# Kernel tuning notes

Measured on AMD Instinct MI355X. Metric: run time of the kernel, lower is better.

The kernel has to match this reference:

```python
import jax, jax.numpy as jnp
import numpy as np

EPS = 1e-5

def layernorm(x, g, b):
    mu = jnp.mean(x, axis=-1, keepdims=True)
    var = jnp.mean((x - mu) ** 2, axis=-1, keepdims=True)
    return (x - mu) * jax.lax.rsqrt(var + EPS) * g + b

def setup_inputs() -> dict:
    key = jax.random.key(0)
    B, T, C, H = 4, 2048, 1024, 16
    hs = C // H  # 64
    ks = jax.random.split(key, 16)
    s_in = 1.0 / np.sqrt(C)
    s_hid = 1.0 / np.sqrt(4 * C)
    return {
        "x":   jax.random.normal(ks[0], (B, T, C), jnp.float32),
        # per-head projections, stacked over heads: [H, C, hs]
        "Wq":  jax.random.normal(ks[1], (H, C, hs), jnp.float32) * s_in,
        "Wk":  jax.random.normal(ks[2], (H, C, hs), jnp.float32) * s_in,
        "Wv":  jax.random.normal(ks[3], (H, C, hs), jnp.float32) * s_in,
        # output projection [C, C] (concat of heads -> C)
        "Wo":  jax.random.normal(ks[4], (C, C), jnp.float32) * s_in,
        "bo":  jnp.zeros((C,), jnp.float32),
        # layernorm params
        "g1":  jnp.ones((C,), jnp.float32),
        "be1": jnp.zeros((C,), jnp.float32),
        "g2":  jnp.ones((C,), jnp.float32),
        "be2": jnp.zeros((C,), jnp.float32),
        # feed-forward: C -> 4C -> C
        "W1":  jax.random.normal(ks[5], (C, 4 * C), jnp.float32) * s_in,
        "b1":  jnp.zeros((4 * C,), jnp.float32),
        "W2":  jax.random.normal(ks[6], (4 * C, C), jnp.float32) * s_hid,
        "b2":  jnp.zeros((C,), jnp.float32),
    }

def reference(x, Wq, Wk, Wv, Wo, bo, g1, be1, g2, be2, W1, b1, W2, b2):
    B, T, C = x.shape
    H, _, hs = Wq.shape
    scale = hs ** -0.5

    # --- self-attention on ln1(x) ---
    xn = layernorm(x, g1, be1)
    q = jnp.einsum('btc,hcd->bhtd', xn, Wq)
    k = jnp.einsum('btc,hcd->bhtd', xn, Wk)
    v = jnp.einsum('btc,hcd->bhtd', xn, Wv)
    scores = jnp.einsum('bhtd,bhsd->bhts', q, k) * scale  # [B,H,T,T]
    causal = jnp.tril(jnp.ones((T, T), dtype=bool))
    scores = jnp.where(causal, scores, jnp.finfo(scores.dtype).min)
    wei = jax.nn.softmax(scores, axis=-1)
    out = jnp.einsum('bhts,bhsd->bhtd', wei, v)           # [B,H,T,hs]
    out = out.transpose(0, 2, 1, 3).reshape(B, T, H * hs)  # concat heads
    x = x + out @ Wo + bo

    # --- feed-forward on ln2(x) ---
    xn2 = layernorm(x, g2, be2)
    h = jax.nn.relu(xn2 @ W1 + b1)
    x = x + h @ W2 + b2
    return x
```

## Files before the change

### kernel.cpp

```cpp
#include <hip/hip_runtime.h>
#include <hip/hip_bf16.h>

typedef __hip_bfloat16 bf16;
typedef __attribute__((ext_vector_type(8))) short bf16x8;
typedef __attribute__((ext_vector_type(4))) short s16x4;
typedef __attribute__((ext_vector_type(4))) float f32x4;

__device__ __forceinline__ float b2f(bf16 v) { return __bfloat162float(v); }
__device__ __forceinline__ bf16  f2b(float v) { return __float2bfloat16(v); }
__device__ __forceinline__ float ldf(const bf16* p)  { return __bfloat162float(*p); }
__device__ __forceinline__ float ldf(const float* p) { return *p; }
__device__ __forceinline__ void  stf(bf16* p, float v)  { *p = __float2bfloat16(v); }
__device__ __forceinline__ void  stf(float* p, float v) { *p = v; }

__device__ __forceinline__ void load_lds16(const bf16* g, short* lds) {
    __builtin_amdgcn_global_load_lds(
        (const __attribute__((address_space(1))) unsigned int*)g,
        (__attribute__((address_space(3))) unsigned int*)lds, 16, 0, 0);
}

template<typename InT>
__global__ __launch_bounds__(256) void ln_kernel(const InT* __restrict__ x,
                                                 const float* __restrict__ g,
                                                 const float* __restrict__ b,
                                                 bf16* __restrict__ out)
{
    const int C = 1024;
    int row = blockIdx.x;
    int tid = threadIdx.x;
    const InT* xr = x + (size_t)row * C;

    float v[4];
    float s = 0.f, s2 = 0.f;
#pragma unroll
    for (int i = 0; i < 4; ++i) {
        float f = ldf(xr + tid + i * 256);
        v[i] = f; s += f; s2 += f * f;
    }
#pragma unroll
    for (int off = 32; off > 0; off >>= 1) {
        s  += __shfl_down(s,  off, 64);
        s2 += __shfl_down(s2, off, 64);
    }
    __shared__ float red[8];
    int wave = tid >> 6;
    if ((tid & 63) == 0) { red[wave] = s; red[wave + 4] = s2; }
    __syncthreads();
    float ts  = red[0] + red[1] + red[2] + red[3];
    float ts2 = red[4] + red[5] + red[6] + red[7];
    float mu  = ts * (1.f / 1024.f);
    float var = ts2 * (1.f / 1024.f) - mu * mu;
    float rstd = rsqrtf(var + 1e-5f);
#pragma unroll
    for (int i = 0; i < 4; ++i) {
        int c = tid + i * 256;
        out[(size_t)row * C + c] = f2b((v[i] - mu) * rstd * g[c] + b[c]);
    }
}

__global__ __launch_bounds__(256) void prep_weights(
    const float* __restrict__ Wq, const float* __restrict__ Wk,
    const float* __restrict__ Wv, const float* __restrict__ Wo,
    const float* __restrict__ W1, const float* __restrict__ W2,
    bf16* __restrict__ wqkvt, bf16* __restrict__ wot,
    bf16* __restrict__ w1t, bf16* __restrict__ w2t)
{
    __shared__ float t[32][33];
    int tx = threadIdx.x & 31, ty = threadIdx.x >> 5;
    int id = blockIdx.x;
    const float* in; bf16* out; int in_ld, out_ld, n0, k0;
    if (id < 3072) {
        const float* Ws[3] = {Wq, Wk, Wv};
        int m = id >> 10, r = id & 1023;
        int z = r >> 6, rt = r & 63;
        in = Ws[m] + z * 65536;
        out = wqkvt + (size_t)(m * 1024 + z * 64) * 1024;
        in_ld = 64; out_ld = 1024;
        n0 = (rt & 1) * 32; k0 = (rt >> 1) * 32;
    } else if (id < 4096) {
        int r = id - 3072;
        in = Wo; out = wot; in_ld = 1024; out_ld = 1024;
        n0 = (r & 31) * 32; k0 = (r >> 5) * 32;
    } else if (id < 8192) {
        int r = id - 4096;
        in = W1; out = w1t; in_ld = 4096; out_ld = 1024;
        n0 = (r & 127) * 32; k0 = (r >> 7) * 32;
    } else {
        int r = id - 8192;
        in = W2; out = w2t; in_ld = 1024; out_ld = 4096;
        n0 = (r & 31) * 32; k0 = (r >> 5) * 32;
    }
#pragma unroll
    for (int i = 0; i < 4; ++i)
        t[ty + i * 8][tx] = in[(size_t)(k0 + ty + i * 8) * in_ld + n0 + tx];
    __syncthreads();
#pragma unroll
    for (int i = 0; i < 4; ++i)
        out[(size_t)(n0 + ty + i * 8) * out_ld + k0 + tx] = f2b(t[tx][ty + i * 8]);
}

__global__ __launch_bounds__(256) void vt_kernel(
    const bf16* __restrict__ qkv, bf16* __restrict__ vt, int T)
{
    __shared__ float t[32][33];
    int tx = threadIdx.x & 31, ty = threadIdx.x >> 5;
    int z = blockIdx.z, b = z >> 4, h = z & 15;
    const bf16* in = qkv + (size_t)b * T * 3072 + 2048 + h * 64;
    bf16* out = vt + (size_t)z * 64 * T;
    int n0 = blockIdx.x * 32, k0 = blockIdx.y * 32;
#pragma unroll
    for (int i = 0; i < 4; ++i)
        t[ty + i * 8][tx] = b2f(in[(size_t)(k0 + ty + i * 8) * 3072 + n0 + tx]);
    __syncthreads();
#pragma unroll
    for (int i = 0; i < 4; ++i)
        out[(size_t)(n0 + ty + i * 8) * T + k0 + tx] = f2b(t[tx][ty + i * 8]);
}

template<bool RELU, bool HAS_BIAS, bool HAS_RES, typename ResT, typename OutT>
__global__ __launch_bounds__(256) void gemm_bt(
    const bf16* __restrict__ A, int lda,
    const bf16* __restrict__ Bt, int ldb,
    const float* __restrict__ bias,
    const ResT* __restrict__ res, int ldr,
    OutT* __restrict__ Cm, int ldc,
    int M, int N, int K)
{
    __shared__ short As[2][128 * 32];
    __shared__ short Bs[2][128 * 32];
    int tid = threadIdx.x, wv = tid >> 6, ln = tid & 63;

    int f = blockIdx.x + blockIdx.y * gridDim.x;
    int nby = gridDim.y;
    int by = f % nby, bx = f / nby;
    int bm0 = by * 128, bn0 = bx * 128;

    int wm = (wv & 1) * 64, wn = (wv >> 1) * 64;
    int quad = ln >> 4, lane15 = ln & 15;

    f32x4 acc[4][4] = {};

    int srow = ln >> 2;
    int scol = (((ln & 3) ^ (srow & 3)) * 8);
    int sw   = (quad ^ (lane15 & 3)) * 8;
    const bf16* Ab = A + (size_t)bm0 * lda;
    const bf16* Bb = Bt + (size_t)bn0 * ldb;

#pragma unroll
    for (int i = 0; i < 2; ++i) {
        int ch = wv + i * 4;
        load_lds16(Ab + (size_t)(ch * 16 + srow) * lda + scol, &As[0][ch * 16 * 32]);
        load_lds16(Bb + (size_t)(ch * 16 + srow) * ldb + scol, &Bs[0][ch * 16 * 32]);
    }
    __syncthreads();

    int cur = 0;
    for (int k0 = 0; k0 < K; k0 += 32) {
        if (k0 + 32 < K) {
            int nb = cur ^ 1;
#pragma unroll
            for (int i = 0; i < 2; ++i) {
                int ch = wv + i * 4;
                load_lds16(Ab + (size_t)(ch * 16 + srow) * lda + k0 + 32 + scol,
                           &As[nb][ch * 16 * 32]);
                load_lds16(Bb + (size_t)(ch * 16 + srow) * ldb + k0 + 32 + scol,
                           &Bs[nb][ch * 16 * 32]);
            }
        }
        bf16x8 af[4], bfr[4];
#pragma unroll
        for (int mi = 0; mi < 4; ++mi)
            af[mi] = *(const bf16x8*)&As[cur][(wm + mi * 16 + lane15) * 32 + sw];
#pragma unroll
        for (int ni = 0; ni < 4; ++ni)
            bfr[ni] = *(const bf16x8*)&Bs[cur][(wn + ni * 16 + lane15) * 32 + sw];
#pragma unroll
        for (int mi = 0; mi < 4; ++mi)
#pragma unroll
            for (int ni = 0; ni < 4; ++ni)
                acc[mi][ni] = __builtin_amdgcn_mfma_f32_16x16x32_bf16(
                    af[mi], bfr[ni], acc[mi][ni], 0, 0, 0);
        __syncthreads();
        cur ^= 1;
    }

#pragma unroll
    for (int mi = 0; mi < 4; ++mi) {
#pragma unroll
        for (int r = 0; r < 4; ++r) {
            int gm = bm0 + wm + mi * 16 + quad * 4 + r;
#pragma unroll
            for (int ni = 0; ni < 4; ++ni) {
                int gn = bn0 + wn + ni * 16 + lane15;
                float v = acc[mi][ni][r];
                if (HAS_BIAS) v += bias[gn];
                if (HAS_RES)  v += ldf(res + (size_t)gm * ldr + gn);
                if (RELU)     v = fmaxf(v, 0.f);
                stf(Cm + (size_t)gm * ldc + gn, v);
            }
        }
    }
}

__device__ __forceinline__ void attn_tile_q(
    const short* __restrict__ Ks, const short* __restrict__ Vs,
    short* __restrict__ Psw,
    const bf16x8* qf, f32x4* oacc, float& mrun, float& lrun,
    int ktbase, int qmin, int quad, int lane15, int r7)
{
    const float scale2 = 0.18033688011112042f;
    const int PS = 72;
    f32x4 sacc[4] = {};
    __builtin_amdgcn_s_setprio(1);
#pragma unroll
    for (int ks = 0; ks < 2; ++ks) {
        int so = ((ks * 4 + quad) ^ r7) * 8;
#pragma unroll
        for (int mi = 0; mi < 4; ++mi) {
            bf16x8 kf = *(const bf16x8*)&Ks[(mi * 16 + lane15) * 64 + so];
            sacc[mi] = __builtin_amdgcn_mfma_f32_16x16x32_bf16(kf, qf[ks], sacc[mi], 0, 0, 0);
        }
    }
    __builtin_amdgcn_s_setprio(0);

    if (ktbase + 63 > qmin) {
        int ql = qmin + lane15;
#pragma unroll
        for (int mi = 0; mi < 4; ++mi)
#pragma unroll
            for (int r = 0; r < 4; ++r)
                if (ktbase + mi * 16 + quad * 4 + r > ql) sacc[mi][r] = -3e38f;
    }

    float mx = sacc[0][0];
#pragma unroll
    for (int mi = 0; mi < 4; ++mi)
#pragma unroll
        for (int r = 0; r < 4; ++r) mx = fmaxf(mx, sacc[mi][r]);
    mx = fmaxf(mx, __shfl_xor(mx, 16, 64));
    mx = fmaxf(mx, __shfl_xor(mx, 32, 64));
    float pmax = mx * scale2;

    if (!__all(pmax <= mrun + 11.5f)) {
        float mn = fmaxf(mrun, pmax);
        float alpha = exp2f(mrun - mn);
        mrun = mn;
        lrun *= alpha;
#pragma unroll
        for (int di = 0; di < 4; ++di)
#pragma unroll
            for (int r = 0; r < 4; ++r) oacc[di][r] *= alpha;
    }

    float psum = 0.f;
#pragma unroll
    for (int mi = 0; mi < 4; ++mi) {
        float p[4];
#pragma unroll
        for (int r = 0; r < 4; ++r) {
            p[r] = exp2f(fmaf(sacc[mi][r], scale2, -mrun));
            psum += p[r];
        }
        short tmp[4];
#pragma unroll
        for (int r = 0; r < 4; ++r) {
            bf16 pb = f2b(p[r]);
            tmp[r] = *(short*)&pb;
        }
        *(s16x4*)&Psw[lane15 * PS + mi * 16 + quad * 4] = *(s16x4*)tmp;
    }
    lrun += psum;

    __builtin_amdgcn_s_setprio(1);
#pragma unroll
    for (int ks = 0; ks < 2; ++ks) {
        int so = ((ks * 4 + quad) ^ r7) * 8;
        bf16x8 pf = *(const bf16x8*)&Psw[lane15 * PS + ks * 32 + quad * 8];
#pragma unroll
        for (int di = 0; di < 4; ++di) {
            bf16x8 vf = *(const bf16x8*)&Vs[(di * 16 + lane15) * 64 + so];
            oacc[di] = __builtin_amdgcn_mfma_f32_16x16x32_bf16(vf, pf, oacc[di], 0, 0, 0);
        }
    }
    __builtin_amdgcn_s_setprio(0);
}

__global__ __launch_bounds__(512, 4) void attn_kernel(
    const bf16* __restrict__ qkv, const bf16* __restrict__ vt,
    bf16* __restrict__ o, int T)
{
    const int LDQ = 3072;
    const int PS = 72;
    int bx = blockIdx.x;
    int qta = 15 - bx;
    int qtb = bx;
    int h = blockIdx.y, b = blockIdx.z;
    int tid = threadIdx.x, wv = tid >> 6, ln = tid & 63;
    int quad = ln >> 4, lane15 = ln & 15, r7 = lane15 & 7;

    __shared__ short KV[2][2][64 * 64];
    __shared__ short Ps[2][8][16 * PS];

    int lr = ln >> 3;
    int lc = ((ln & 7) ^ lr) * 8;

    const bf16* kbase = qkv + (size_t)(b * T) * LDQ + 1024 + h * 64;
    const bf16* vbase = vt + (size_t)((b * 16 + h) * 64) * T;

#pragma unroll
    for (int i = 0; i < 2; ++i) {
        int ch = wv * 2 + i;
        load_lds16(qkv + (size_t)(b * T + qta * 128 + ch * 8 + lr) * LDQ + h * 64 + lc,
                   &KV[0][0][ch * 512]);
        load_lds16(qkv + (size_t)(b * T + qtb * 128 + ch * 8 + lr) * LDQ + h * 64 + lc,
                   &KV[1][0][ch * 512]);
    }
    __syncthreads();
    bf16x8 qfa[2], qfb[2];
#pragma unroll
    for (int ks = 0; ks < 2; ++ks) {
        int off = (wv * 16 + lane15) * 64 + (((ks * 4 + quad) ^ r7) * 8);
        qfa[ks] = *(const bf16x8*)&KV[0][0][off];
        qfb[ks] = *(const bf16x8*)&KV[1][0][off];
    }
    __syncthreads();

    f32x4 oacca[4] = {}, oaccb[4] = {};
    float mra = -1e30f, lra = 0.f, mrb = -1e30f, lrb = 0.f;
    int qmina = qta * 128 + wv * 16;
    int qminb = qtb * 128 + wv * 16;
    int ntiles = 2 * qta + 2;

    load_lds16(kbase + (size_t)(wv * 8 + lr) * LDQ + lc, &KV[0][0][wv * 8 * 64]);
    load_lds16(vbase + (size_t)(wv * 8 + lr) * T + lc, &KV[0][1][wv * 8 * 64]);

    for (int kt = 0; kt < ntiles; ++kt) {
        __syncthreads();
        if (kt + 1 < ntiles) {
            int nb = (kt + 1) & 1;
            load_lds16(kbase + (size_t)((kt + 1) * 64 + wv * 8 + lr) * LDQ + lc,
                       &KV[nb][0][wv * 8 * 64]);
            load_lds16(vbase + (size_t)(wv * 8 + lr) * T + (kt + 1) * 64 + lc,
                       &KV[nb][1][wv * 8 * 64]);
        }
        const short* Ks = &KV[kt & 1][0][0];
        const short* Vs = &KV[kt & 1][1][0];
        int kb = kt * 64;

        if (kb <= qmina + 15)
            attn_tile_q(Ks, Vs, &Ps[0][wv][0], qfa, oacca, mra, lra,
                        kb, qmina, quad, lane15, r7);
        if (kb <= qminb + 15)
            attn_tile_q(Ks, Vs, &Ps[1][wv][0], qfb, oaccb, mrb, lrb,
                        kb, qminb, quad, lane15, r7);
    }

    lra += __shfl_xor(lra, 16, 64);
    lra += __shfl_xor(lra, 32, 64);
    float inva = 1.f / lra;
    size_t rowa = (size_t)(b * T + qta * 128 + wv * 16 + lane15);
#pragma unroll
    for (int di = 0; di < 4; ++di) {
        short tmp[4];
#pragma unroll
        for (int r = 0; r < 4; ++r) {
            bf16 ob = f2b(oacca[di][r] * inva);
            tmp[r] = *(short*)&ob;
        }
        *(s16x4*)&o[rowa * 1024 + h * 64 + di * 16 + quad * 4] = *(s16x4*)tmp;
    }

    lrb += __shfl_xor(lrb, 16, 64);
    lrb += __shfl_xor(lrb, 32, 64);
    float invb = 1.f / lrb;
    size_t rowb = (size_t)(b * T + qtb * 128 + wv * 16 + lane15);
#pragma unroll
    for (int di = 0; di < 4; ++di) {
        short tmp[4];
#pragma unroll
        for (int r = 0; r < 4; ++r) {
            bf16 ob = f2b(oaccb[di][r] * invb);
            tmp[r] = *(short*)&ob;
        }
        *(s16x4*)&o[rowb * 1024 + h * 64 + di * 16 + quad * 4] = *(s16x4*)tmp;
    }
}

extern "C" void kernel_launch(void* const* d_in, const int* in_sizes, int n_in,
                              void* d_out, int out_size, void* d_ws, size_t ws_size,
                              hipStream_t stream)
{
    (void)in_sizes; (void)n_in; (void)out_size; (void)ws_size;
    const float* x   = (const float*)d_in[0];
    const float* Wq  = (const float*)d_in[1];
    const float* Wk  = (const float*)d_in[2];
    const float* Wv  = (const float*)d_in[3];
    const float* Wo  = (const float*)d_in[4];
    const float* bo  = (const float*)d_in[5];
    const float* g1  = (const float*)d_in[6];
    const float* be1 = (const float*)d_in[7];
    const float* g2  = (const float*)d_in[8];
    const float* be2 = (const float*)d_in[9];
    const float* W1  = (const float*)d_in[10];
    const float* b1  = (const float*)d_in[11];
    const float* W2  = (const float*)d_in[12];
    const float* b2  = (const float*)d_in[13];

    const int T = 2048, M = 4 * T;
    const size_t MB = 1ull << 20;
    char* ws = (char*)d_ws;

    bf16*  xn    = (bf16*)(ws + 0 * MB);
    bf16*  qkv   = (bf16*)(ws + 16 * MB);
    bf16*  vt    = (bf16*)(ws + 64 * MB);
    bf16*  wqkvt = (bf16*)(ws + 80 * MB);
    bf16*  x1b   = (bf16*)(ws + 80 * MB);
    bf16*  wot   = (bf16*)(ws + 96 * MB);
    bf16*  xn2   = (bf16*)(ws + 96 * MB);
    bf16*  w1t   = (bf16*)(ws + 112 * MB);
    bf16*  w2t   = (bf16*)(ws + 120 * MB);
    bf16*  attnb = (bf16*)(ws + 0 * MB);
    bf16*  hb    = (bf16*)(ws + 0 * MB);

    dim3 blk(256);

    prep_weights<<<12288, blk, 0, stream>>>(Wq, Wk, Wv, Wo, W1, W2,
                                            wqkvt, wot, w1t, w2t);

    ln_kernel<float><<<M, blk, 0, stream>>>(x, g1, be1, xn);

    gemm_bt<false, false, false, float, bf16><<<dim3(24, 64), blk, 0, stream>>>(
        xn, 1024, wqkvt, 1024, nullptr, nullptr, 0, qkv, 3072, M, 3072, 1024);

    vt_kernel<<<dim3(2, T / 32, 64), blk, 0, stream>>>(qkv, vt, T);

    attn_kernel<<<dim3(8, 16, 4), dim3(512), 0, stream>>>(qkv, vt, attnb, T);

    gemm_bt<false, true, true, float, bf16><<<dim3(8, 64), blk, 0, stream>>>(
        attnb, 1024, wot, 1024, bo, x, 1024, x1b, 1024, M, 1024, 1024);

    ln_kernel<bf16><<<M, blk, 0, stream>>>(x1b, g2, be2, xn2);

    gemm_bt<true, true, false, float, bf16><<<dim3(32, 64), blk, 0, stream>>>(
        xn2, 1024, w1t, 1024, b1, nullptr, 0, hb, 4096, M, 4096, 1024);

    gemm_bt<false, true, true, bf16, float><<<dim3(8, 64), blk, 0, stream>>>(
        hb, 4096, w2t, 4096, b2, x1b, 1024, (float*)d_out, 1024, M, 1024, 4096);
}
```

Before: 504.8 us.

## Add BK=64 GEMM tile for FFN down-proj, fix LDS swizzle, vectorize layernorm

The GEMM gains a K-tile template parameter. The K=4096 down-projection now uses a 64-wide K tile with an 8-way XOR swizzle, which halves the number of loop iterations and barriers per output tile. The BK=32 swizzle is also changed to a different XOR pattern to reduce LDS bank conflicts on fragment reads. Layernorm switches to vectorized float4/bf16x4 loads and stores with a contiguous per-thread column mapping, and the larger tile doubles LDS use for that GEMM.

```diff
diff --git a/kernel.cpp b/kernel.cpp
--- a/kernel.cpp
+++ b/kernel.cpp
@@ -13,6 +13,16 @@
 __device__ __forceinline__ void  stf(bf16* p, float v)  { *p = __float2bfloat16(v); }
 __device__ __forceinline__ void  stf(float* p, float v) { *p = v; }
 
+__device__ __forceinline__ void ld4(const float* p, float* v) {
+    float4 t = *(const float4*)p;
+    v[0] = t.x; v[1] = t.y; v[2] = t.z; v[3] = t.w;
+}
+__device__ __forceinline__ void ld4(const bf16* p, float* v) {
+    s16x4 t = *(const s16x4*)p;
+#pragma unroll
+    for (int j = 0; j < 4; ++j) { short s = t[j]; v[j] = b2f(*(bf16*)&s); }
+}
+
 __device__ __forceinline__ void load_lds16(const bf16* g, short* lds) {
     __builtin_amdgcn_global_load_lds(
         (const __attribute__((address_space(1))) unsigned int*)g,
@@ -31,12 +41,10 @@
     const InT* xr = x + (size_t)row * C;
 
     float v[4];
+    ld4(xr + tid * 4, v);
     float s = 0.f, s2 = 0.f;
 #pragma unroll
-    for (int i = 0; i < 4; ++i) {
-        float f = ldf(xr + tid + i * 256);
-        v[i] = f; s += f; s2 += f * f;
-    }
+    for (int i = 0; i < 4; ++i) { s += v[i]; s2 += v[i] * v[i]; }
 #pragma unroll
     for (int off = 32; off > 0; off >>= 1) {
         s  += __shfl_down(s,  off, 64);
@@ -51,11 +59,18 @@
     float mu  = ts * (1.f / 1024.f);
     float var = ts2 * (1.f / 1024.f) - mu * mu;
     float rstd = rsqrtf(var + 1e-5f);
-#pragma unroll
-    for (int i = 0; i < 4; ++i) {
-        int c = tid + i * 256;
-        out[(size_t)row * C + c] = f2b((v[i] - mu) * rstd * g[c] + b[c]);
-    }
+
+    float4 gg = *(const float4*)(g + tid * 4);
+    float4 bb = *(const float4*)(b + tid * 4);
+    float gj[4] = {gg.x, gg.y, gg.z, gg.w};
+    float bj[4] = {bb.x, bb.y, bb.z, bb.w};
+    s16x4 o4;
+#pragma unroll
+    for (int j = 0; j < 4; ++j) {
+        bf16 ob = f2b((v[j] - mu) * rstd * gj[j] + bj[j]);
+        o4[j] = *(short*)&ob;
+    }
+    *(s16x4*)(out + (size_t)row * C + tid * 4) = o4;
 }
 
 __global__ __launch_bounds__(256) void prep_weights(
@@ -117,7 +132,7 @@
         out[(size_t)(n0 + ty + i * 8) * T + k0 + tx] = f2b(t[tx][ty + i * 8]);
 }
 
-template<bool RELU, bool HAS_BIAS, bool HAS_RES, typename ResT, typename OutT>
+template<int BK, bool RELU, bool HAS_BIAS, bool HAS_RES, typename ResT, typename OutT>
 __global__ __launch_bounds__(256) void gemm_bt(
     const bf16* __restrict__ A, int lda,
     const bf16* __restrict__ Bt, int ldb,
@@ -126,8 +141,8 @@
     OutT* __restrict__ Cm, int ldc,
     int M, int N, int K)
 {
-    __shared__ short As[2][128 * 32];
-    __shared__ short Bs[2][128 * 32];
+    __shared__ short As[2][128 * BK];
+    __shared__ short Bs[2][128 * BK];
     int tid = threadIdx.x, wv = tid >> 6, ln = tid & 63;
 
     int f = blockIdx.x + blockIdx.y * gridDim.x;
@@ -140,46 +155,75 @@
 
     f32x4 acc[4][4] = {};
 
-    int srow = ln >> 2;
-    int scol = (((ln & 3) ^ (srow & 3)) * 8);
-    int sw   = (quad ^ (lane15 & 3)) * 8;
     const bf16* Ab = A + (size_t)bm0 * lda;
     const bf16* Bb = Bt + (size_t)bn0 * ldb;
 
-#pragma unroll
-    for (int i = 0; i < 2; ++i) {
-        int ch = wv + i * 4;
-        load_lds16(Ab + (size_t)(ch * 16 + srow) * lda + scol, &As[0][ch * 16 * 32]);
-        load_lds16(Bb + (size_t)(ch * 16 + srow) * ldb + scol, &Bs[0][ch * 16 * 32]);
-    }
-    __syncthreads();
-
-    int cur = 0;
-    for (int k0 = 0; k0 < K; k0 += 32) {
-        if (k0 + 32 < K) {
-            int nb = cur ^ 1;
+    auto stage = [&](int buf, int kk) {
+        if constexpr (BK == 32) {
+            int srow = ln >> 2;
+            int scol = (((ln & 3) ^ ((ln >> 3) & 3)) * 8);
 #pragma unroll
             for (int i = 0; i < 2; ++i) {
                 int ch = wv + i * 4;
-                load_lds16(Ab + (size_t)(ch * 16 + srow) * lda + k0 + 32 + scol,
-                           &As[nb][ch * 16 * 32]);
-                load_lds16(Bb + (size_t)(ch * 16 + srow) * ldb + k0 + 32 + scol,
-                           &Bs[nb][ch * 16 * 32]);
+                load_lds16(Ab + (size_t)(ch * 16 + srow) * lda + kk + scol,
+                           &As[buf][ch * 16 * 32]);
+                load_lds16(Bb + (size_t)(ch * 16 + srow) * ldb + kk + scol,
+                           &Bs[buf][ch * 16 * 32]);
             }
-        }
-        bf16x8 af[4], bfr[4];
-#pragma unroll
-        for (int mi = 0; mi < 4; ++mi)
-            af[mi] = *(const bf16x8*)&As[cur][(wm + mi * 16 + lane15) * 32 + sw];
-#pragma unroll
-        for (int ni = 0; ni < 4; ++ni)
-            bfr[ni] = *(const bf16x8*)&Bs[cur][(wn + ni * 16 + lane15) * 32 + sw];
-#pragma unroll
-        for (int mi = 0; mi < 4; ++mi)
+        } else {
+            int srow = ln >> 3;
+            int scol = ((ln & 7) ^ srow) * 8;
+#pragma unroll
+            for (int i = 0; i < 4; ++i) {
+                int r0 = i * 32 + wv * 8;
+                load_lds16(Ab + (size_t)(r0 + srow) * lda + kk + scol,
+                           &As[buf][r0 * 64]);
+                load_lds16(Bb + (size_t)(r0 + srow) * ldb + kk + scol,
+                           &Bs[buf][r0 * 64]);
+            }
+        }
+    };
+
+    stage(0, 0);
+    __syncthreads();
+
+    int cur = 0;
+    for (int k0 = 0; k0 < K; k0 += BK) {
+        if (k0 + BK < K) stage(cur ^ 1, k0 + BK);
+        if constexpr (BK == 32) {
+            int sw = (quad ^ ((lane15 >> 1) & 3)) * 8;
+            bf16x8 af[4], bfr[4];
+#pragma unroll
+            for (int mi = 0; mi < 4; ++mi)
+                af[mi] = *(const bf16x8*)&As[cur][(wm + mi * 16 + lane15) * 32 + sw];
 #pragma unroll
             for (int ni = 0; ni < 4; ++ni)
-                acc[mi][ni] = __builtin_amdgcn_mfma_f32_16x16x32_bf16(
-                    af[mi], bfr[ni], acc[mi][ni], 0, 0, 0);
+                bfr[ni] = *(const bf16x8*)&Bs[cur][(wn + ni * 16 + lane15) * 32 + sw];
+#pragma unroll
+            for (int mi = 0; mi < 4; ++mi)
+#pragma unroll
+                for (int ni = 0; ni < 4; ++ni)
+                    acc[mi][ni] = __builtin_amdgcn_mfma_f32_16x16x32_bf16(
+                        af[mi], bfr[ni], acc[mi][ni], 0, 0, 0);
+        } else {
+#pragma unroll
+            for (int ks = 0; ks < 2; ++ks) {
+                int sw = (((ks * 4 + quad) ^ (lane15 & 7)) * 8);
+                bf16x8 af[4], bfr[4];
+#pragma unroll
+                for (int mi = 0; mi < 4; ++mi)
+                    af[mi] = *(const bf16x8*)&As[cur][(wm + mi * 16 + lane15) * 64 + sw];
+#pragma unroll
+                for (int ni = 0; ni < 4; ++ni)
+                    bfr[ni] = *(const bf16x8*)&Bs[cur][(wn + ni * 16 + lane15) * 64 + sw];
+#pragma unroll
+                for (int mi = 0; mi < 4; ++mi)
+#pragma unroll
+                    for (int ni = 0; ni < 4; ++ni)
+                        acc[mi][ni] = __builtin_amdgcn_mfma_f32_16x16x32_bf16(
+                            af[mi], bfr[ni], acc[mi][ni], 0, 0, 0);
+            }
+        }
         __syncthreads();
         cur ^= 1;
     }
@@ -429,21 +473,21 @@
 
     ln_kernel<float><<<M, blk, 0, stream>>>(x, g1, be1, xn);
 
-    gemm_bt<false, false, false, float, bf16><<<dim3(24, 64), blk, 0, stream>>>(
+    gemm_bt<32, false, false, false, float, bf16><<<dim3(24, 64), blk, 0, stream>>>(
         xn, 1024, wqkvt, 1024, nullptr, nullptr, 0, qkv, 3072, M, 3072, 1024);
 
     vt_kernel<<<dim3(2, T / 32, 64), blk, 0, stream>>>(qkv, vt, T);
 
     attn_kernel<<<dim3(8, 16, 4), dim3(512), 0, stream>>>(qkv, vt, attnb, T);
 
-    gemm_bt<false, true, true, float, bf16><<<dim3(8, 64), blk, 0, stream>>>(
+    gemm_bt<32, false, true, true, float, bf16><<<dim3(8, 64), blk, 0, stream>>>(
         attnb, 1024, wot, 1024, bo, x, 1024, x1b, 1024, M, 1024, 1024);
 
     ln_kernel<bf16><<<M, blk, 0, stream>>>(x1b, g2, be2, xn2);
 
-    gemm_bt<true, true, false, float, bf16><<<dim3(32, 64), blk, 0, stream>>>(
+    gemm_bt<32, true, true, false, float, bf16><<<dim3(32, 64), blk, 0, stream>>>(
         xn2, 1024, w1t, 1024, b1, nullptr, 0, hb, 4096, M, 4096, 1024);
 
-    gemm_bt<false, true, true, bf16, float><<<dim3(8, 64), blk, 0, stream>>>(
+    gemm_bt<64, false, true, true, bf16, float><<<dim3(8, 64), blk, 0, stream>>>(
         hb, 4096, w2t, 4096, b2, x1b, 1024, (float*)d_out, 1024, M, 1024, 4096);
 }
```

Result: faster. 488.3 us (-3.3%).
